# Kernel tuning notes

Hardware: AMD Instinct MI355X
Metric: run time of the kernel (lower is better)

Reference implementation:

```python
import jax, jax.numpy as jnp
import numpy as np

ATT_LEN = 128  # must match init att_len


def setup_inputs() -> dict:
    key = jax.random.key(0)
    ks = jax.random.split(key, 6)
    B, T, U, L = 64, 4096, 512, ATT_LEN
    s = 1.0 / np.sqrt(U)
    return {
        "query": jax.random.normal(ks[0], (B, U), jnp.float32),
        "values": jax.random.normal(ks[1], (B, T, U), jnp.float32),
        "pos": jax.random.randint(ks[2], (B,), 0, T, jnp.int32),
        "W1": jax.random.normal(ks[3], (U, U), jnp.float32) * s,
        "b1": jnp.zeros((U,), jnp.float32),
        "W2": jax.random.normal(ks[4], (U, U), jnp.float32) * s,
        "b2": jnp.zeros((U,), jnp.float32),
        "V": jax.random.normal(ks[5], (U, 1), jnp.float32) * s,
        "bV": jnp.zeros((1,), jnp.float32),
    }


def _gather_windows(values, pos, att_len):
    """Vectorized version of the TF while_loop: per-example window of
    length att_len around pos, zero-padded where it runs off either end."""
    B, T, U = values.shape
    half = att_len // 2
    start = jnp.maximum(pos - half, 0)            # [B]
    end = jnp.minimum(pos + half, T)              # [B]
    xlen = end - start                            # [B]
    offs = jnp.arange(att_len, dtype=pos.dtype)   # [L]
    idx = start[:, None] + offs[None, :]          # [B, L]
    mask = offs[None, :] < xlen[:, None]          # [B, L] valid (unpadded) slots
    safe_idx = jnp.clip(idx, 0, T - 1)
    gathered = jnp.take_along_axis(values, safe_idx[:, :, None], axis=1)  # [B, L, U]
    values_att = jnp.where(mask[:, :, None], gathered, jnp.zeros((), values.dtype))
    xpos = jnp.where(mask, idx.astype(values.dtype), 0.0)  # [B, L]
    return values_att, xpos


def reference(query, values, pos, W1, b1, W2, b2, V, bV):
    values_att, _xpos = _gather_windows(values, pos, ATT_LEN)  # [B, L, U]
    # score = V(tanh(W1(values_att) + W2(query)[:, None, :]))
    h = jnp.tanh(jnp.einsum('blu,uv->blv', values_att, W1) + b1
                 + (query @ W2 + b2)[:, None, :])              # [B, L, U]
    score = jnp.einsum('blu,uo->blo', h, V) + bV               # [B, L, 1]
    attention_weights = jax.nn.softmax(score, axis=1)          # [B, L, 1]
    context_vector = jnp.sum(attention_weights * values_att, axis=1)  # [B, U]
    return context_vector, attention_weights
```

## Files before the change

kernel.cpp:

```cpp
#include <hip/hip_runtime.h>
#include <math.h>

#define NB 64
#define NT 4096
#define NU 512
#define NL 128
#define HALF 64

typedef __bf16 bf16x8 __attribute__((ext_vector_type(8)));
typedef float f32x4 __attribute__((ext_vector_type(4)));

__device__ inline unsigned short f2bf(float f) {
    unsigned u = __float_as_uint(f);
    u += 0x7fff + ((u >> 16) & 1);
    return (unsigned short)(u >> 16);
}

__device__ inline float tanh_fast(float x) {
    float xc = fminf(15.f, fmaxf(-15.f, x));
    float t = __expf(2.f * xc);
    return (t - 1.f) * __builtin_amdgcn_rcpf(t + 1.f);
}

__global__ __launch_bounds__(256) void k_prepA(const float* __restrict__ query,
                                               const float* __restrict__ values,
                                               const int* __restrict__ pos,
                                               const float* __restrict__ W1,
                                               const float* __restrict__ b1,
                                               const float* __restrict__ W2,
                                               const float* __restrict__ b2,
                                               float* __restrict__ q2,
                                               unsigned short* __restrict__ W1T,
                                               unsigned short* __restrict__ Gb) {
    __shared__ float sh[1056];
    const int blk = blockIdx.x, tid = threadIdx.x;

    if (blk < 256) {
        const int b = blk >> 2, cq = blk & 3;
        sh[tid]       = query[b * NU + tid];
        sh[tid + 256] = query[b * NU + tid + 256];
        __syncthreads();
        const int col  = cq * 128 + (tid & 127);
        const int half = tid >> 7;
        const float* wp = W2 + (size_t)(half * 256) * NU + col;
        float a = 0.f;
        #pragma unroll 8
        for (int uu = 0; uu < 256; ++uu)
            a = fmaf(sh[half * 256 + uu], wp[(size_t)uu * NU], a);
        if (half == 0) sh[512 + (tid & 127)] = a;
        __syncthreads();
        if (half == 1)
            q2[(size_t)b * NU + col] = a + sh[512 + (tid & 127)] + b1[col] + b2[col];
    } else if (blk < 512) {
        const int t  = blk - 256;
        const int tr = t >> 4, tc = t & 15;
        const int cc = tid & 31, r0 = tid >> 5;
        #pragma unroll
        for (int i = 0; i < 4; ++i) {
            const int r = r0 + i * 8;
            sh[r * 33 + cc] = W1[(size_t)(tr * 32 + r) * NU + tc * 32 + cc];
        }
        __syncthreads();
        #pragma unroll
        for (int i = 0; i < 4; ++i) {
            const int r = r0 + i * 8;
            W1T[(size_t)(tc * 32 + r) * NU + tr * 32 + cc] = f2bf(sh[cc * 33 + r]);
        }
    } else {
        const int g = blk - 512;
        #pragma unroll
        for (int i = 0; i < 8; ++i) {
            const int c   = tid + i * 256;
            const int rl  = c >> 7;
            const int off = (c & 127) * 4;
            const int rg  = g * 16 + rl;
            const int b   = rg >> 7, l = rg & 127;
            const int p     = pos[b];
            const int start = max(p - HALF, 0);
            const int xlen  = min(p + HALF, NT) - start;
            float4 v = make_float4(0.f, 0.f, 0.f, 0.f);
            if (l < xlen)
                v = *(const float4*)&values[((size_t)(b * NT + start + l)) * NU + off];
            uint2 pk;
            pk.x = f2bf(v.x) | ((unsigned)f2bf(v.y) << 16);
            pk.y = f2bf(v.z) | ((unsigned)f2bf(v.w) << 16);
            *(uint2*)&Gb[(size_t)rg * NU + off] = pk;
        }
    }
}

__global__ __launch_bounds__(256, 2) void k_score6(const unsigned short* __restrict__ Gb,
                                                   const unsigned short* __restrict__ W1T,
                                                   const float* __restrict__ q2,
                                                   const float* __restrict__ V,
                                                   float* __restrict__ part) {
    __shared__ unsigned short As[64 * 64];
    __shared__ unsigned short Bs[128 * 64];
    __shared__ float pl[64][2];

    const int id = blockIdx.x;
    const int nb = id >> 7, rb = id & 127;
    const int b  = rb >> 1, l0 = (rb & 1) * 64, n0 = nb * 128;
    const int tid = threadIdx.x, lane = tid & 63, w = tid >> 6;
    const int wr = w >> 1, wc = w & 1;

    const unsigned short* Asrc = Gb + ((size_t)(b * NL + l0)) * NU;
    const unsigned short* Bsrc = W1T + (size_t)n0 * NU;

    f32x4 acc[2][4];
    #pragma unroll
    for (int m = 0; m < 2; ++m)
        #pragma unroll
        for (int n = 0; n < 4; ++n) acc[m][n] = (f32x4){0.f, 0.f, 0.f, 0.f};

    for (int k0 = 0; k0 < NU; k0 += 64) {
        #pragma unroll
        for (int i = 0; i < 2; ++i) {
            const int c   = tid + i * 256;
            const int row = c >> 3, ch = c & 7;
            uint4 v = *(const uint4*)&Asrc[(size_t)row * NU + k0 + ch * 8];
            *(uint4*)((char*)As + row * 128 + ((ch * 16) ^ ((row & 7) << 4))) = v;
        }
        #pragma unroll
        for (int i = 0; i < 4; ++i) {
            const int c   = tid + i * 256;
            const int col = c >> 3, ch = c & 7;
            uint4 v = *(const uint4*)&Bsrc[(size_t)col * NU + k0 + ch * 8];
            *(uint4*)((char*)Bs + col * 128 + ((ch * 16) ^ ((col & 7) << 4))) = v;
        }
        __syncthreads();

        #pragma unroll
        for (int kh = 0; kh < 2; ++kh) {
            const int koff = kh * 64 + (lane >> 4) * 16;
            bf16x8 af[2];
            #pragma unroll
            for (int m = 0; m < 2; ++m) {
                const int rowA = wr * 32 + m * 16 + (lane & 15);
                af[m] = *(const bf16x8*)((const char*)As + rowA * 128 + (koff ^ ((rowA & 7) << 4)));
            }
            #pragma unroll
            for (int n = 0; n < 4; ++n) {
                const int colB = wc * 64 + n * 16 + (lane & 15);
                const bf16x8 bf = *(const bf16x8*)((const char*)Bs + colB * 128 + (koff ^ ((colB & 7) << 4)));
                #pragma unroll
                for (int m = 0; m < 2; ++m)
                    acc[m][n] = __builtin_amdgcn_mfma_f32_16x16x32_bf16(af[m], bf, acc[m][n], 0, 0, 0);
            }
        }
        __syncthreads();
    }

    float partial[2][4];
    #pragma unroll
    for (int m = 0; m < 2; ++m)
        #pragma unroll
        for (int r = 0; r < 4; ++r) partial[m][r] = 0.f;

    #pragma unroll
    for (int n = 0; n < 4; ++n) {
        const int col = n0 + wc * 64 + n * 16 + (lane & 15);
        const float qq = q2[(size_t)b * NU + col];
        const float vv = V[col];
        #pragma unroll
        for (int m = 0; m < 2; ++m)
            #pragma unroll
            for (int r = 0; r < 4; ++r)
                partial[m][r] += tanh_fast(acc[m][n][r] + qq) * vv;
    }
    #pragma unroll
    for (int off = 1; off < 16; off <<= 1)
        #pragma unroll
        for (int m = 0; m < 2; ++m)
            #pragma unroll
            for (int r = 0; r < 4; ++r)
                partial[m][r] += __shfl_xor(partial[m][r], off, 16);

    if ((lane & 15) == 0) {
        #pragma unroll
        for (int m = 0; m < 2; ++m)
            #pragma unroll
            for (int r = 0; r < 4; ++r)
                pl[wr * 32 + m * 16 + ((lane >> 4) << 2) + r][wc] = partial[m][r];
    }
    __syncthreads();

    if (tid < 64)
        part[((size_t)nb * NB + b) * NL + l0 + tid] = pl[tid][0] + pl[tid][1];
}

__global__ __launch_bounds__(256) void k_ctx2(const float* __restrict__ values,
                                              const int* __restrict__ pos,
                                              const float* __restrict__ part,
                                              const float* __restrict__ bV,
                                              float* __restrict__ out) {
    const int b = blockIdx.x, uq = blockIdx.y, tid = threadIdx.x;
    __shared__ float wsm[NL];
    __shared__ float red[4];
    __shared__ float cp[128];

    float s = -1e30f;
    if (tid < NL) {
        s = bV[0];
        #pragma unroll
        for (int nb = 0; nb < 4; ++nb) s += part[((size_t)nb * NB + b) * NL + tid];
    }
    float m = s;
    #pragma unroll
    for (int off = 32; off >= 1; off >>= 1) m = fmaxf(m, __shfl_xor(m, off, 64));
    if (tid < NL && (tid & 63) == 0) red[tid >> 6] = m;
    __syncthreads();
    const float M = fmaxf(red[0], red[1]);
    const float e = (tid < NL) ? __expf(s - M) : 0.f;
    float t = e;
    #pragma unroll
    for (int off = 32; off >= 1; off >>= 1) t += __shfl_xor(t, off, 64);
    if (tid < NL && (tid & 63) == 0) red[2 + (tid >> 6)] = t;
    __syncthreads();
    const float S = red[2] + red[3];
    if (tid < NL) {
        const float wv = e / S;
        wsm[tid] = wv;
        if (uq == 0) out[NB * NU + b * NL + tid] = wv;
    }
    __syncthreads();

    const int p     = pos[b];
    const int start = max(p - HALF, 0);
    const int xlen  = min(p + HALF, NT) - start;
    const float* vbase = values + ((size_t)b * NT + start) * NU;

    const int u    = uq * 128 + (tid & 127);
    const int half = tid >> 7;
    const int lbeg = half * 64;
    const int lend = min(xlen, lbeg + 64);
    float a = 0.f;
    #pragma unroll 4
    for (int l = lbeg; l < lend; ++l)
        a = fmaf(wsm[l], vbase[(size_t)l * NU + u], a);

    if (half == 0) cp[tid] = a;
    __syncthreads();
    if (half == 1) out[b * NU + u] = cp[tid & 127] + a;
}

#define BM 64
#define BN 128
#define BK 64
#define ASTRIDE 68

__global__ __launch_bounds__(256) void k_q2(const float* __restrict__ query,
                                            const float* __restrict__ W2,
                                            const float* __restrict__ b2,
                                            const float* __restrict__ b1,
                                            float* __restrict__ q2) {
    const int b = blockIdx.x, tid = threadIdx.x;
    __shared__ float qs[NU];
    qs[tid]       = query[b * NU + tid];
    qs[tid + 256] = query[b * NU + tid + 256];
    __syncthreads();
    float a0 = 0.f, a1 = 0.f;
    const float* w = W2 + tid;
    #pragma unroll 8
    for (int u = 0; u < NU; ++u) {
        const float q = qs[u];
        a0 = fmaf(q, w[(size_t)u * NU], a0);
        a1 = fmaf(q, w[(size_t)u * NU + 256], a1);
    }
    q2[b * NU + tid]       = a0 + b2[tid] + b1[tid];
    q2[b * NU + tid + 256] = a1 + b2[tid + 256] + b1[tid + 256];
}

__global__ __launch_bounds__(256) void k_score(const float* __restrict__ values,
                                               const int* __restrict__ pos,
                                               const float* __restrict__ W1,
                                               const float* __restrict__ V,
                                               const float* __restrict__ q2,
                                               float* __restrict__ part) {
    __shared__ float As2[BK][ASTRIDE];
    __shared__ float Bs2[BK][BN];
    const int rb = blockIdx.x, nb = blockIdx.y;
    const int b  = rb >> 1;
    const int l0 = (rb & 1) * BM;
    const int n0 = nb * BN;
    const int tid = threadIdx.x;
    const int tx = tid & 15, ty = tid >> 4;
    const int p     = pos[b];
    const int start = max(p - HALF, 0);
    const int xlen  = min(p + HALF, NT) - start;
    const float* vbase = values + ((size_t)b * NT + start) * NU;

    float acc[4][8];
    #pragma unroll
    for (int r = 0; r < 4; ++r)
        #pragma unroll
        for (int c = 0; c < 8; ++c) acc[r][c] = 0.f;

    for (int k0 = 0; k0 < NU; k0 += BK) {
        #pragma unroll
        for (int i = 0; i < 4; ++i) {
            const int f = tid + i * 256;
            const int row = f >> 4, kq = f & 15;
            const int l = l0 + row;
            float4 v4 = make_float4(0.f, 0.f, 0.f, 0.f);
            if (l < xlen)
                v4 = *(const float4*)&vbase[(size_t)l * NU + k0 + kq * 4];
            As2[kq * 4 + 0][row] = v4.x;
            As2[kq * 4 + 1][row] = v4.y;
            As2[kq * 4 + 2][row] = v4.z;
            As2[kq * 4 + 3][row] = v4.w;
        }
        #pragma unroll
        for (int i = 0; i < 8; ++i) {
            const int f = tid + i * 256;
            const int kk = f >> 5, nq = f & 31;
            *(float4*)&Bs2[kk][nq * 4] =
                *(const float4*)&W1[(size_t)(k0 + kk) * NU + n0 + nq * 4];
        }
        __syncthreads();
        #pragma unroll 16
        for (int kk = 0; kk < BK; ++kk) {
            const float4 a  = *(const float4*)&As2[kk][ty * 4];
            const float4 b0 = *(const float4*)&Bs2[kk][tx * 8];
            const float4 b1v = *(const float4*)&Bs2[kk][tx * 8 + 4];
            const float av[4] = {a.x, a.y, a.z, a.w};
            const float bv[8] = {b0.x, b0.y, b0.z, b0.w, b1v.x, b1v.y, b1v.z, b1v.w};
            #pragma unroll
            for (int r = 0; r < 4; ++r)
                #pragma unroll
                for (int c = 0; c < 8; ++c)
                    acc[r][c] = fmaf(av[r], bv[c], acc[r][c]);
        }
        __syncthreads();
    }
    float partial[4] = {0.f, 0.f, 0.f, 0.f};
    #pragma unroll
    for (int c = 0; c < 8; ++c) {
        const int v = n0 + tx * 8 + c;
        const float vv = V[v];
        const float qq = q2[b * NU + v];
        #pragma unroll
        for (int r = 0; r < 4; ++r)
            partial[r] += tanhf(acc[r][c] + qq) * vv;
    }
    #pragma unroll
    for (int off = 1; off < 16; off <<= 1)
        #pragma unroll
        for (int r = 0; r < 4; ++r)
            partial[r] += __shfl_xor(partial[r], off, 16);
    if (tx == 0) {
        #pragma unroll
        for (int r = 0; r < 4; ++r) {
            const int l = l0 + ty * 4 + r;
            part[((size_t)nb * NB + b) * NL + l] = partial[r];
        }
    }
}

__global__ __launch_bounds__(256) void k_ctx(const float* __restrict__ values,
                                             const int* __restrict__ pos,
                                             const float* __restrict__ part,
                                             const float* __restrict__ bV,
                                             float* __restrict__ out) {
    const int b = blockIdx.x, tid = threadIdx.x;
    __shared__ float wsh[NL];
    __shared__ float red2[4];

    float s = -1e30f;
    if (tid < NL) {
        s = bV[0];
        #pragma unroll
        for (int nb = 0; nb < 4; ++nb) s += part[((size_t)nb * NB + b) * NL + tid];
    }
    float m = s;
    #pragma unroll
    for (int off = 32; off >= 1; off >>= 1) m = fmaxf(m, __shfl_xor(m, off, 64));
    if (tid < NL && (tid & 63) == 0) red2[tid >> 6] = m;
    __syncthreads();
    const float M = fmaxf(red2[0], red2[1]);
    const float e = (tid < NL) ? expf(s - M) : 0.f;
    float t = e;
    #pragma unroll
    for (int off = 32; off >= 1; off >>= 1) t += __shfl_xor(t, off, 64);
    if (tid < NL && (tid & 63) == 0) red2[2 + (tid >> 6)] = t;
    __syncthreads();
    const float S = red2[2] + red2[3];
    if (tid < NL) wsh[tid] = e / S;
    __syncthreads();

    if (tid < NL) out[NB * NU + b * NL + tid] = wsh[tid];

    const int p     = pos[b];
    const int start = max(p - HALF, 0);
    const int xlen  = min(p + HALF, NT) - start;
    const float* vb = values + ((size_t)b * NT + start) * NU;

    float a0 = 0.f, a1 = 0.f;
    for (int l = 0; l < xlen; ++l) {
        const float wl = wsh[l];
        a0 = fmaf(wl, vb[(size_t)l * NU + tid], a0);
        a1 = fmaf(wl, vb[(size_t)l * NU + tid + 256], a1);
    }
    out[b * NU + tid]       = a0;
    out[b * NU + tid + 256] = a1;
}

extern "C" void kernel_launch(void* const* d_in, const int* in_sizes, int n_in,
                              void* d_out, int out_size, void* d_ws, size_t ws_size,
                              hipStream_t stream) {
    const float* query  = (const float*)d_in[0];
    const float* values = (const float*)d_in[1];
    const int*   pos    = (const int*)d_in[2];
    const float* W1     = (const float*)d_in[3];
    const float* b1     = (const float*)d_in[4];
    const float* W2     = (const float*)d_in[5];
    const float* b2     = (const float*)d_in[6];
    const float* V      = (const float*)d_in[7];
    const float* bV     = (const float*)d_in[8];
    float* out = (float*)d_out;

    const size_t need = 131072u + 131072u + 524288u + 8388608u;
    if (ws_size >= need) {
        float* q2            = (float*)d_ws;
        float* part          = (float*)((char*)d_ws + 131072);
        unsigned short* W1T  = (unsigned short*)((char*)d_ws + 262144);
        unsigned short* Gb   = (unsigned short*)((char*)d_ws + 786432);
        k_prepA<<<1024, 256, 0, stream>>>(query, values, pos, W1, b1, W2, b2, q2, W1T, Gb);
        k_score6<<<512, 256, 0, stream>>>(Gb, W1T, q2, V, part);
        k_ctx2<<<dim3(NB, 4), 256, 0, stream>>>(values, pos, part, bV, out);
    } else {
        float* q2   = (float*)d_ws;
        float* part = (float*)((char*)d_ws + 131072);
        k_q2<<<NB, 256, 0, stream>>>(query, W2, b2, b1, q2);
        k_score<<<dim3(NB * NL / BM, NU / BN), 256, 0, stream>>>(values, pos, W1, V, q2, part);
        k_ctx<<<NB, 256, 0, stream>>>(values, pos, part, bV, out);
    }
}
```

Before: 38.38 us.

## Use 128x128 score tiles with intra-block split-K across 8 waves

The score GEMM kernel now runs 256 blocks of 512 threads, each computing a full 128-row by 128-column tile for one batch element instead of a 64x128 tile. The eight waves split the K dimension in two halves per 64-wide chunk and reduce their accumulators through shared memory before the tanh and V projection epilogue. The block-to-batch mapping is also remapped so neighbouring blocks share W1 columns. This aims to halve redundant W1 tile loads and raise MFMA work per LDS load, at the cost of extra barriers, an LDS reduction pass, and fewer blocks (256 on a GPU with 256 CUs), which may limit latency hiding.

```diff
diff --git a/kernel.cpp b/kernel.cpp
--- a/kernel.cpp
+++ b/kernel.cpp
@@ -89,104 +89,143 @@
     }
 }
 
-__global__ __launch_bounds__(256, 2) void k_score6(const unsigned short* __restrict__ Gb,
-                                                   const unsigned short* __restrict__ W1T,
-                                                   const float* __restrict__ q2,
-                                                   const float* __restrict__ V,
-                                                   float* __restrict__ part) {
-    __shared__ unsigned short As[64 * 64];
-    __shared__ unsigned short Bs[128 * 64];
-    __shared__ float pl[64][2];
+__global__ __launch_bounds__(512, 2) void k_score10(const unsigned short* __restrict__ Gb,
+                                                    const unsigned short* __restrict__ W1T,
+                                                    const float* __restrict__ q2,
+                                                    const float* __restrict__ V,
+                                                    float* __restrict__ part) {
+    __shared__ unsigned short AB[256 * 64];
+    __shared__ float pl[NL][2];
+
+    unsigned short* As = AB;
+    unsigned short* Bs = AB + 128 * 64;
+    float* buf = (float*)AB;
 
     const int id = blockIdx.x;
-    const int nb = id >> 7, rb = id & 127;
-    const int b  = rb >> 1, l0 = (rb & 1) * 64, n0 = nb * 128;
+    const int tt = id >> 3;
+    const int b  = (tt >> 2) * 8 + (id & 7);
+    const int nb = tt & 3;
+    const int n0 = nb * 128;
     const int tid = threadIdx.x, lane = tid & 63, w = tid >> 6;
-    const int wr = w >> 1, wc = w & 1;
-
-    const unsigned short* Asrc = Gb + ((size_t)(b * NL + l0)) * NU;
+    const int wr = w & 1, wc = (w >> 1) & 1, kh = w >> 2;
+
+    const unsigned short* Asrc = Gb + (size_t)b * NL * NU;
     const unsigned short* Bsrc = W1T + (size_t)n0 * NU;
 
-    f32x4 acc[2][4];
-    #pragma unroll
-    for (int m = 0; m < 2; ++m)
+    f32x4 acc[4][4];
+    #pragma unroll
+    for (int m = 0; m < 4; ++m)
         #pragma unroll
         for (int n = 0; n < 4; ++n) acc[m][n] = (f32x4){0.f, 0.f, 0.f, 0.f};
 
+    const int koff = kh * 64 + (lane >> 4) * 16;
+
     for (int k0 = 0; k0 < NU; k0 += 64) {
         #pragma unroll
         for (int i = 0; i < 2; ++i) {
-            const int c   = tid + i * 256;
+            const int c   = tid + i * 512;
             const int row = c >> 3, ch = c & 7;
             uint4 v = *(const uint4*)&Asrc[(size_t)row * NU + k0 + ch * 8];
             *(uint4*)((char*)As + row * 128 + ((ch * 16) ^ ((row & 7) << 4))) = v;
         }
         #pragma unroll
-        for (int i = 0; i < 4; ++i) {
-            const int c   = tid + i * 256;
+        for (int i = 0; i < 2; ++i) {
+            const int c   = tid + i * 512;
             const int col = c >> 3, ch = c & 7;
             uint4 v = *(const uint4*)&Bsrc[(size_t)col * NU + k0 + ch * 8];
             *(uint4*)((char*)Bs + col * 128 + ((ch * 16) ^ ((col & 7) << 4))) = v;
         }
         __syncthreads();
 
-        #pragma unroll
-        for (int kh = 0; kh < 2; ++kh) {
-            const int koff = kh * 64 + (lane >> 4) * 16;
-            bf16x8 af[2];
-            #pragma unroll
-            for (int m = 0; m < 2; ++m) {
-                const int rowA = wr * 32 + m * 16 + (lane & 15);
-                af[m] = *(const bf16x8*)((const char*)As + rowA * 128 + (koff ^ ((rowA & 7) << 4)));
+        bf16x8 af[4];
+        #pragma unroll
+        for (int m = 0; m < 4; ++m) {
+            const int rowA = wr * 64 + m * 16 + (lane & 15);
+            af[m] = *(const bf16x8*)((const char*)As + rowA * 128 + (koff ^ ((rowA & 7) << 4)));
+        }
+        #pragma unroll
+        for (int n = 0; n < 4; ++n) {
+            const int colB = wc * 64 + n * 16 + (lane & 15);
+            const bf16x8 bf = *(const bf16x8*)((const char*)Bs + colB * 128 + (koff ^ ((colB & 7) << 4)));
+            #pragma unroll
+            for (int m = 0; m < 4; ++m)
+                acc[m][n] = __builtin_amdgcn_mfma_f32_16x16x32_bf16(af[m], bf, acc[m][n], 0, 0, 0);
+        }
+        __syncthreads();
+    }
+
+    #pragma unroll
+    for (int r = 0; r < 2; ++r) {
+        if (kh == 1 && wr == r) {
+            #pragma unroll
+            for (int m = 0; m < 4; ++m) {
+                const int lrow = m * 16 + ((lane >> 4) << 2);
+                #pragma unroll
+                for (int n = 0; n < 4; ++n) {
+                    const int col = wc * 64 + n * 16 + (lane & 15);
+                    #pragma unroll
+                    for (int j = 0; j < 4; ++j)
+                        buf[(lrow + j) * 128 + col] = acc[m][n][j];
+                }
             }
-            #pragma unroll
-            for (int n = 0; n < 4; ++n) {
-                const int colB = wc * 64 + n * 16 + (lane & 15);
-                const bf16x8 bf = *(const bf16x8*)((const char*)Bs + colB * 128 + (koff ^ ((colB & 7) << 4)));
-                #pragma unroll
-                for (int m = 0; m < 2; ++m)
-                    acc[m][n] = __builtin_amdgcn_mfma_f32_16x16x32_bf16(af[m], bf, acc[m][n], 0, 0, 0);
+        }
+        __syncthreads();
+        if (kh == 0 && wr == r) {
+            #pragma unroll
+            for (int m = 0; m < 4; ++m) {
+                const int lrow = m * 16 + ((lane >> 4) << 2);
+                #pragma unroll
+                for (int n = 0; n < 4; ++n) {
+                    const int col = wc * 64 + n * 16 + (lane & 15);
+                    #pragma unroll
+                    for (int j = 0; j < 4; ++j)
+                        acc[m][n][j] += buf[(lrow + j) * 128 + col];
+                }
             }
         }
         __syncthreads();
     }
 
-    float partial[2][4];
-    #pragma unroll
-    for (int m = 0; m < 2; ++m)
-        #pragma unroll
-        for (int r = 0; r < 4; ++r) partial[m][r] = 0.f;
-
-    #pragma unroll
-    for (int n = 0; n < 4; ++n) {
-        const int col = n0 + wc * 64 + n * 16 + (lane & 15);
-        const float qq = q2[(size_t)b * NU + col];
-        const float vv = V[col];
-        #pragma unroll
-        for (int m = 0; m < 2; ++m)
-            #pragma unroll
-            for (int r = 0; r < 4; ++r)
-                partial[m][r] += tanh_fast(acc[m][n][r] + qq) * vv;
-    }
-    #pragma unroll
-    for (int off = 1; off < 16; off <<= 1)
-        #pragma unroll
-        for (int m = 0; m < 2; ++m)
-            #pragma unroll
-            for (int r = 0; r < 4; ++r)
-                partial[m][r] += __shfl_xor(partial[m][r], off, 16);
-
-    if ((lane & 15) == 0) {
-        #pragma unroll
-        for (int m = 0; m < 2; ++m)
-            #pragma unroll
-            for (int r = 0; r < 4; ++r)
-                pl[wr * 32 + m * 16 + ((lane >> 4) << 2) + r][wc] = partial[m][r];
-    }
-    __syncthreads();
-
-    if (tid < 64)
-        part[((size_t)nb * NB + b) * NL + l0 + tid] = pl[tid][0] + pl[tid][1];
+    if (kh == 0) {
+        float partial[4][4];
+        #pragma unroll
+        for (int m = 0; m < 4; ++m)
+            #pragma unroll
+            for (int j = 0; j < 4; ++j) partial[m][j] = 0.f;
+
+        #pragma unroll
+        for (int n = 0; n < 4; ++n) {
+            const int col = n0 + wc * 64 + n * 16 + (lane & 15);
+            const float qq = q2[(size_t)b * NU + col];
+            const float vv = V[col];
+            #pragma unroll
+            for (int m = 0; m < 4; ++m)
+                #pragma unroll
+                for (int j = 0; j < 4; ++j)
+                    partial[m][j] += tanh_fast(acc[m][n][j] + qq) * vv;
+        }
+        #pragma unroll
+        for (int off = 1; off < 16; off <<= 1)
+            #pragma unroll
+            for (int m = 0; m < 4; ++m)
+                #pragma unroll
+                for (int j = 0; j < 4; ++j)
+                    partial[m][j] += __shfl_xor(partial[m][j], off, 16);
+
+        if ((lane & 15) == 0) {
+            #pragma unroll
+            for (int m = 0; m < 4; ++m)
+                #pragma unroll
+                for (int j = 0; j < 4; ++j) {
+                    const int row = wr * 64 + m * 16 + ((lane >> 4) << 2) + j;
+                    pl[row][wc] = partial[m][j];
+                }
+        }
+    }
+    __syncthreads();
+
+    if (tid < NL)
+        part[((size_t)nb * NB + b) * NL + tid] = pl[tid][0] + pl[tid][1];
 }
 
 __global__ __launch_bounds__(256) void k_ctx2(const float* __restrict__ values,
@@ -426,7 +465,7 @@
         unsigned short* W1T  = (unsigned short*)((char*)d_ws + 262144);
         unsigned short* Gb   = (unsigned short*)((char*)d_ws + 786432);
         k_prepA<<<1024, 256, 0, stream>>>(query, values, pos, W1, b1, W2, b2, q2, W1T, Gb);
-        k_score6<<<512, 256, 0, stream>>>(Gb, W1T, q2, V, part);
+        k_score10<<<256, 512, 0, stream>>>(Gb, W1T, q2, V, part);
         k_ctx2<<<dim3(NB, 4), 256, 0, stream>>>(values, pos, part, bV, out);
     } else {
         float* q2   = (float*)d_ws;
```

Measured after the change: 40.28 us. +5.0%, slower.

## Fuse softmax and context reduction into score kernel via last-block atomics

Applied to the files above, without the earlier changes.

Removes the separate context kernel launch. The score kernel counts finished tiles per batch with an atomic counter, and the last block computes the softmax and publishes the weights with a release flag. Even-row blocks spin on that flag and then compute their slice of the context vector. This saves one launch and its tail, but adds spin-waiting that depends on all eight blocks per batch being co-resident or already finished, which risks deadlock or stalls.

```diff
diff --git a/kernel.cpp b/kernel.cpp
--- a/kernel.cpp
+++ b/kernel.cpp
@@ -31,7 +31,9 @@
                                                const float* __restrict__ b2,
                                                float* __restrict__ q2,
                                                unsigned short* __restrict__ W1T,
-                                               unsigned short* __restrict__ Gb) {
+                                               unsigned short* __restrict__ Gb,
+                                               int* __restrict__ cnt,
+                                               int* __restrict__ flag) {
     __shared__ float sh[1056];
     const int blk = blockIdx.x, tid = threadIdx.x;
 
@@ -67,6 +69,7 @@
             W1T[(size_t)(tc * 32 + r) * NU + tr * 32 + cc] = f2bf(sh[cc * 33 + r]);
         }
     } else {
+        if (blk == 512 && tid < NB) { cnt[tid] = 0; flag[tid] = 0; }
         const int g = blk - 512;
         #pragma unroll
         for (int i = 0; i < 8; ++i) {
@@ -89,14 +92,25 @@
     }
 }
 
-__global__ __launch_bounds__(256, 2) void k_score6(const unsigned short* __restrict__ Gb,
-                                                   const unsigned short* __restrict__ W1T,
-                                                   const float* __restrict__ q2,
-                                                   const float* __restrict__ V,
-                                                   float* __restrict__ part) {
+__global__ __launch_bounds__(256, 2) void k_score11(const unsigned short* __restrict__ Gb,
+                                                    const unsigned short* __restrict__ W1T,
+                                                    const float* __restrict__ q2,
+                                                    const float* __restrict__ V,
+                                                    const float* __restrict__ values,
+                                                    const int* __restrict__ pos,
+                                                    const float* __restrict__ bV,
+                                                    float* __restrict__ part,
+                                                    int* __restrict__ cnt,
+                                                    int* __restrict__ flag,
+                                                    float* __restrict__ wsmG,
+                                                    float* __restrict__ out) {
     __shared__ unsigned short As[64 * 64];
     __shared__ unsigned short Bs[128 * 64];
     __shared__ float pl[64][2];
+    __shared__ float wsmS[NL];
+    __shared__ float red[4];
+    __shared__ float cp[128];
+    __shared__ int amLastSh;
 
     const int id = blockIdx.x;
     const int nb = id >> 7, rb = id & 127;
@@ -185,63 +199,78 @@
     }
     __syncthreads();
 
-    if (tid < 64)
+    if (tid < 64) {
         part[((size_t)nb * NB + b) * NL + l0 + tid] = pl[tid][0] + pl[tid][1];
-}
-
-__global__ __launch_bounds__(256) void k_ctx2(const float* __restrict__ values,
-                                              const int* __restrict__ pos,
-                                              const float* __restrict__ part,
-                                              const float* __restrict__ bV,
-                                              float* __restrict__ out) {
-    const int b = blockIdx.x, uq = blockIdx.y, tid = threadIdx.x;
-    __shared__ float wsm[NL];
-    __shared__ float red[4];
-    __shared__ float cp[128];
-
-    float s = -1e30f;
-    if (tid < NL) {
-        s = bV[0];
-        #pragma unroll
-        for (int nb = 0; nb < 4; ++nb) s += part[((size_t)nb * NB + b) * NL + tid];
-    }
-    float m = s;
-    #pragma unroll
-    for (int off = 32; off >= 1; off >>= 1) m = fmaxf(m, __shfl_xor(m, off, 64));
-    if (tid < NL && (tid & 63) == 0) red[tid >> 6] = m;
-    __syncthreads();
-    const float M = fmaxf(red[0], red[1]);
-    const float e = (tid < NL) ? __expf(s - M) : 0.f;
-    float t = e;
-    #pragma unroll
-    for (int off = 32; off >= 1; off >>= 1) t += __shfl_xor(t, off, 64);
-    if (tid < NL && (tid & 63) == 0) red[2 + (tid >> 6)] = t;
-    __syncthreads();
-    const float S = red[2] + red[3];
-    if (tid < NL) {
-        const float wv = e / S;
-        wsm[tid] = wv;
-        if (uq == 0) out[NB * NU + b * NL + tid] = wv;
-    }
-    __syncthreads();
-
-    const int p     = pos[b];
-    const int start = max(p - HALF, 0);
-    const int xlen  = min(p + HALF, NT) - start;
-    const float* vbase = values + ((size_t)b * NT + start) * NU;
-
-    const int u    = uq * 128 + (tid & 127);
-    const int half = tid >> 7;
-    const int lbeg = half * 64;
-    const int lend = min(xlen, lbeg + 64);
-    float a = 0.f;
-    #pragma unroll 4
-    for (int l = lbeg; l < lend; ++l)
-        a = fmaf(wsm[l], vbase[(size_t)l * NU + u], a);
-
-    if (half == 0) cp[tid] = a;
-    __syncthreads();
-    if (half == 1) out[b * NU + u] = cp[tid & 127] + a;
+        __threadfence();
+    }
+    __syncthreads();
+    if (tid == 0)
+        amLastSh = (atomicAdd(&cnt[b], 1) == 7);
+    __syncthreads();
+
+    if (amLastSh) {
+        float s = -1e30f;
+        if (tid < NL) {
+            s = bV[0];
+            #pragma unroll
+            for (int q = 0; q < 4; ++q)
+                s += __hip_atomic_load(&part[((size_t)q * NB + b) * NL + tid],
+                                       __ATOMIC_RELAXED, __HIP_MEMORY_SCOPE_AGENT);
+        }
+        float m = s;
+        #pragma unroll
+        for (int off = 32; off >= 1; off >>= 1) m = fmaxf(m, __shfl_xor(m, off, 64));
+        if (tid < NL && (tid & 63) == 0) red[tid >> 6] = m;
+        __syncthreads();
+        const float M = fmaxf(red[0], red[1]);
+        const float e = (tid < NL) ? __expf(s - M) : 0.f;
+        float t = e;
+        #pragma unroll
+        for (int off = 32; off >= 1; off >>= 1) t += __shfl_xor(t, off, 64);
+        if (tid < NL && (tid & 63) == 0) red[2 + (tid >> 6)] = t;
+        __syncthreads();
+        const float S = red[2] + red[3];
+        if (tid < NL) {
+            const float wv = e / S;
+            wsmG[(size_t)b * NL + tid] = wv;
+            out[NB * NU + b * NL + tid] = wv;
+        }
+        __threadfence();
+        __syncthreads();
+        if (tid == 0)
+            __hip_atomic_store(&flag[b], 1, __ATOMIC_RELEASE, __HIP_MEMORY_SCOPE_AGENT);
+    }
+
+    if ((rb & 1) == 0) {
+        if (tid == 0) {
+            while (__hip_atomic_load(&flag[b], __ATOMIC_ACQUIRE,
+                                     __HIP_MEMORY_SCOPE_AGENT) == 0)
+                __builtin_amdgcn_s_sleep(8);
+        }
+        __syncthreads();
+        if (tid < NL)
+            wsmS[tid] = __hip_atomic_load(&wsmG[(size_t)b * NL + tid],
+                                          __ATOMIC_RELAXED, __HIP_MEMORY_SCOPE_AGENT);
+        __syncthreads();
+
+        const int p     = pos[b];
+        const int start = max(p - HALF, 0);
+        const int xlen  = min(p + HALF, NT) - start;
+        const float* vbase = values + ((size_t)b * NT + start) * NU;
+
+        const int u    = nb * 128 + (tid & 127);
+        const int half = tid >> 7;
+        const int lbeg = half * 64;
+        const int lend = min(xlen, lbeg + 64);
+        float a = 0.f;
+        #pragma unroll 4
+        for (int l = lbeg; l < lend; ++l)
+            a = fmaf(wsmS[l], vbase[(size_t)l * NU + u], a);
+
+        if (half == 0) cp[tid] = a;
+        __syncthreads();
+        if (half == 1) out[b * NU + u] = cp[tid & 127] + a;
+    }
 }
 
 #define BM 64
@@ -419,15 +448,20 @@
     const float* bV     = (const float*)d_in[8];
     float* out = (float*)d_out;
 
-    const size_t need = 131072u + 131072u + 524288u + 8388608u;
+    const size_t offCnt  = 131072u + 131072u + 524288u + 8388608u;
+    const size_t need    = offCnt + 256u + 256u + 32768u;
     if (ws_size >= need) {
         float* q2            = (float*)d_ws;
         float* part          = (float*)((char*)d_ws + 131072);
         unsigned short* W1T  = (unsigned short*)((char*)d_ws + 262144);
         unsigned short* Gb   = (unsigned short*)((char*)d_ws + 786432);
-        k_prepA<<<1024, 256, 0, stream>>>(query, values, pos, W1, b1, W2, b2, q2, W1T, Gb);
-        k_score6<<<512, 256, 0, stream>>>(Gb, W1T, q2, V, part);
-        k_ctx2<<<dim3(NB, 4), 256, 0, stream>>>(values, pos, part, bV, out);
+        int* cnt             = (int*)((char*)d_ws + offCnt);
+        int* flag            = (int*)((char*)d_ws + offCnt + 256);
+        float* wsmG          = (float*)((char*)d_ws + offCnt + 512);
+        k_prepA<<<1024, 256, 0, stream>>>(query, values, pos, W1, b1, W2, b2,
+                                          q2, W1T, Gb, cnt, flag);
+        k_score11<<<512, 256, 0, stream>>>(Gb, W1T, q2, V, values, pos, bV,
+                                           part, cnt, flag, wsmG, out);
     } else {
         float* q2   = (float*)d_ws;
         float* part = (float*)((char*)d_ws + 131072);
```

Result: slower. 70.34 us (+83.3%).

## Fuse score and context kernels via cooperative launch with grid sync

Applied to the files above, without the earlier changes.

Merges the score GEMM kernel and the softmax/context kernel into one cooperative kernel with a grid-wide barrier between them. After the barrier, each of the 512 blocks recomputes the softmax for its batch row and builds a 64-wide slice of the context vector, so the separate kernel launch disappears. The cost is a grid.sync, redundant softmax work in every block, and a dependence on all 512 blocks being co-resident (2 per CU). It also leaves dead code behind (an unused variable and an empty if-block).

```diff
diff --git a/kernel.cpp b/kernel.cpp
--- a/kernel.cpp
+++ b/kernel.cpp
@@ -1,5 +1,8 @@
 #include <hip/hip_runtime.h>
+#include <hip/hip_cooperative_groups.h>
 #include <math.h>
+
+namespace cg = cooperative_groups;
 
 #define NB 64
 #define NT 4096
@@ -89,14 +92,21 @@
     }
 }
 
-__global__ __launch_bounds__(256, 2) void k_score6(const unsigned short* __restrict__ Gb,
-                                                   const unsigned short* __restrict__ W1T,
-                                                   const float* __restrict__ q2,
-                                                   const float* __restrict__ V,
-                                                   float* __restrict__ part) {
+__global__ __launch_bounds__(256, 2) void k_scctx(const unsigned short* __restrict__ Gb,
+                                                  const unsigned short* __restrict__ W1T,
+                                                  const float* __restrict__ q2,
+                                                  const float* __restrict__ V,
+                                                  const float* __restrict__ values,
+                                                  const int* __restrict__ pos,
+                                                  const float* __restrict__ bV,
+                                                  float* __restrict__ part,
+                                                  float* __restrict__ out) {
     __shared__ unsigned short As[64 * 64];
     __shared__ unsigned short Bs[128 * 64];
     __shared__ float pl[64][2];
+    __shared__ float wsm[NL];
+    __shared__ float red[4];
+    __shared__ float cp[4][64];
 
     const int id = blockIdx.x;
     const int nb = id >> 7, rb = id & 127;
@@ -185,25 +195,20 @@
     }
     __syncthreads();
 
-    if (tid < 64)
+    if (tid < 64) {
         part[((size_t)nb * NB + b) * NL + l0 + tid] = pl[tid][0] + pl[tid][1];
-}
-
-__global__ __launch_bounds__(256) void k_ctx2(const float* __restrict__ values,
-                                              const int* __restrict__ pos,
-                                              const float* __restrict__ part,
-                                              const float* __restrict__ bV,
-                                              float* __restrict__ out) {
-    const int b = blockIdx.x, uq = blockIdx.y, tid = threadIdx.x;
-    __shared__ float wsm[NL];
-    __shared__ float red[4];
-    __shared__ float cp[128];
+        __threadfence();
+    }
+
+    cg::this_grid().sync();
 
     float s = -1e30f;
     if (tid < NL) {
         s = bV[0];
         #pragma unroll
-        for (int nb = 0; nb < 4; ++nb) s += part[((size_t)nb * NB + b) * NL + tid];
+        for (int q = 0; q < 4; ++q)
+            s += __hip_atomic_load(&part[((size_t)q * NB + b) * NL + tid],
+                                   __ATOMIC_RELAXED, __HIP_MEMORY_SCOPE_AGENT);
     }
     float m = s;
     #pragma unroll
@@ -221,7 +226,8 @@
     if (tid < NL) {
         const float wv = e / S;
         wsm[tid] = wv;
-        if (uq == 0) out[NB * NU + b * NL + tid] = wv;
+        if (id < NB * 2 && (rb & 1) == 0 && nb == 0) {  }
+        if (nb == 0 && (rb & 1) == 0) out[NB * NU + b * NL + tid] = wv;
     }
     __syncthreads();
 
@@ -230,18 +236,20 @@
     const int xlen  = min(p + HALF, NT) - start;
     const float* vbase = values + ((size_t)b * NT + start) * NU;
 
-    const int u    = uq * 128 + (tid & 127);
-    const int half = tid >> 7;
-    const int lbeg = half * 64;
-    const int lend = min(xlen, lbeg + 64);
+    const int u    = n0 + l0  + (lane & 63) - l0 + l0;
+    const int uu   = n0 + (rb & 1) * 64 + lane;
+    const int lbeg = w * 32;
+    const int lend = min(xlen, lbeg + 32);
     float a = 0.f;
     #pragma unroll 4
     for (int l = lbeg; l < lend; ++l)
-        a = fmaf(wsm[l], vbase[(size_t)l * NU + u], a);
-
-    if (half == 0) cp[tid] = a;
-    __syncthreads();
-    if (half == 1) out[b * NU + u] = cp[tid & 127] + a;
+        a = fmaf(wsm[l], vbase[(size_t)l * NU + uu], a);
+    cp[w][lane] = a;
+    __syncthreads();
+    if (tid < 64)
+        out[b * NU + (n0 + (rb & 1) * 64 + tid)] =
+            cp[0][tid] + cp[1][tid] + cp[2][tid] + cp[3][tid];
+    (void)u;
 }
 
 #define BM 64
@@ -426,8 +434,12 @@
         unsigned short* W1T  = (unsigned short*)((char*)d_ws + 262144);
         unsigned short* Gb   = (unsigned short*)((char*)d_ws + 786432);
         k_prepA<<<1024, 256, 0, stream>>>(query, values, pos, W1, b1, W2, b2, q2, W1T, Gb);
-        k_score6<<<512, 256, 0, stream>>>(Gb, W1T, q2, V, part);
-        k_ctx2<<<dim3(NB, 4), 256, 0, stream>>>(values, pos, part, bV, out);
+
+        void* args[] = { (void*)&Gb, (void*)&W1T, (void*)&q2, (void*)&V,
+                         (void*)&values, (void*)&pos, (void*)&bV,
+                         (void*)&part, (void*)&out };
+        hipLaunchCooperativeKernel((void*)k_scctx, dim3(512), dim3(256),
+                                   args, 0, stream);
     } else {
         float* q2   = (float*)d_ws;
         float* part = (float*)((char*)d_ws + 131072);
```

Result: slower. 76.68 us (+99.8%).
